# Kernel optimization log

Measured on AMD Instinct MI355X. Metric: run time of the kernel, lower is better.

Reference implementation:

```python
import jax, jax.numpy as jnp
import numpy as np

WS = 8        # window_size
HEAD_DIM = 32
KEYS = ["ln1_g", "ln1_b", "qkv_w", "qkv_b", "rpb", "proj_w", "proj_b",
        "ln2_g", "ln2_b", "w1", "b1", "w2", "b2"]


def _rel_bias(rpb, ws):
    # rpb: [h, 2ws-1, 2ws-1] -> bias [h, P, P] via relative coordinates
    coords = np.stack(np.meshgrid(np.arange(ws), np.arange(ws), indexing='ij'), -1).reshape(-1, 2)
    rel = coords[:, None, :] - coords[None, :, :] + ws - 1  # [P,P,2]
    return rpb[:, rel[..., 0], rel[..., 1]]


def _sw_mask(nh, nw, p, shift):
    # boolean mask [nW, P, P]; True = masked (cross-segment after cyclic shift)
    m = np.zeros((nh, nw, p, p, p, p), dtype=bool)
    s = p - shift
    m[-1, :, :s, :, s:, :] = True
    m[-1, :, s:, :, :s, :] = True
    m[:, -1, :, :s, :, s:] = True
    m[:, -1, :, s:, :, :s] = True
    return jnp.asarray(m.reshape(nh * nw, p * p, p * p))


def _ln(x, g, b):
    mu = x.mean(-1, keepdims=True)
    var = ((x - mu) ** 2).mean(-1, keepdims=True)
    return (x - mu) / jnp.sqrt(var + 1e-5) * g + b


def _wmsa(x, qkv_w, qkv_b, rpb, proj_w, proj_b, shifted):
    B, H, W, C = x.shape
    ws, hd = WS, HEAD_DIM
    h = C // hd
    shift = ws // 2
    if shifted:
        x = jnp.roll(x, (-shift, -shift), axis=(1, 2))
    nh, nw = H // ws, W // ws
    # window partition: [B, nW, P, C]
    xw = x.reshape(B, nh, ws, nw, ws, C).transpose(0, 1, 3, 2, 4, 5).reshape(B, nh * nw, ws * ws, C)
    qkv = xw @ qkv_w + qkv_b                               # [B,nW,P,3C]
    qkv = qkv.reshape(B, nh * nw, ws * ws, 3, h, hd)       # (3h,c) split -> first h heads = q
    q, k, v = qkv[..., 0, :, :], qkv[..., 1, :, :], qkv[..., 2, :, :]
    sim = jnp.einsum('bwphd,bwqhd->bhwpq', q, k) * (hd ** -0.5)
    sim = sim + _rel_bias(rpb, ws)[None, :, None]
    if shifted:
        mask = _sw_mask(nh, nw, ws, shift)                 # [nW,P,P]
        sim = jnp.where(mask[None, None], -jnp.inf, sim)
    probs = jax.nn.softmax(sim, axis=-1)
    out = jnp.einsum('bhwpq,bwqhd->bwphd', probs, v).reshape(B, nh * nw, ws * ws, C)
    out = out @ proj_w + proj_b
    out = out.reshape(B, nh, nw, ws, ws, C).transpose(0, 1, 3, 2, 4, 5).reshape(B, H, W, C)
    if shifted:
        out = jnp.roll(out, (shift, shift), axis=(1, 2))
    return out


def _block(x, p, shifted):
    x = x + _wmsa(_ln(x, p['ln1_g'], p['ln1_b']), p['qkv_w'], p['qkv_b'], p['rpb'],
                  p['proj_w'], p['proj_b'], shifted)
    y = _ln(x, p['ln2_g'], p['ln2_b'])
    y = jax.nn.gelu(y @ p['w1'] + p['b1'], approximate=False) @ p['w2'] + p['b2']
    return x + y


def setup_inputs() -> dict:
    B, C, H, W = 2, 192, 256, 256
    h = C // HEAD_DIM
    key = jax.random.key(0)
    ks = jax.random.split(key, 11)
    n = lambda k, shape: jax.random.normal(k, shape, jnp.float32) * 0.02
    inp = {"x": jax.random.normal(ks[0], (B, C, H, W), jnp.float32)}
    for i, pre in enumerate(("b1_", "b2_")):
        o = 1 + i * 5
        inp[pre + "ln1_g"] = jnp.ones((C,), jnp.float32)
        inp[pre + "ln1_b"] = jnp.zeros((C,), jnp.float32)
        inp[pre + "qkv_w"] = n(ks[o], (C, 3 * C))
        inp[pre + "qkv_b"] = jnp.zeros((3 * C,), jnp.float32)
        inp[pre + "rpb"] = n(ks[o + 1], (h, 2 * WS - 1, 2 * WS - 1))
        inp[pre + "proj_w"] = n(ks[o + 2], (C, C))
        inp[pre + "proj_b"] = jnp.zeros((C,), jnp.float32)
        inp[pre + "ln2_g"] = jnp.ones((C,), jnp.float32)
        inp[pre + "ln2_b"] = jnp.zeros((C,), jnp.float32)
        inp[pre + "w1"] = n(ks[o + 3], (C, 4 * C))
        inp[pre + "b1"] = jnp.zeros((4 * C,), jnp.float32)
        inp[pre + "w2"] = n(ks[o + 4], (4 * C, C))
        inp[pre + "b2"] = jnp.zeros((C,), jnp.float32)
    return inp


def reference(x, b1_ln1_g, b1_ln1_b, b1_qkv_w, b1_qkv_b, b1_rpb, b1_proj_w, b1_proj_b,
              b1_ln2_g, b1_ln2_b, b1_w1, b1_b1, b1_w2, b1_b2,
              b2_ln1_g, b2_ln1_b, b2_qkv_w, b2_qkv_b, b2_rpb, b2_proj_w, b2_proj_b,
              b2_ln2_g, b2_ln2_b, b2_w1, b2_b1, b2_w2, b2_b2):
    p1 = dict(zip(KEYS, (b1_ln1_g, b1_ln1_b, b1_qkv_w, b1_qkv_b, b1_rpb, b1_proj_w, b1_proj_b,
                         b1_ln2_g, b1_ln2_b, b1_w1, b1_b1, b1_w2, b1_b2)))
    p2 = dict(zip(KEYS, (b2_ln1_g, b2_ln1_b, b2_qkv_w, b2_qkv_b, b2_rpb, b2_proj_w, b2_proj_b,
                         b2_ln2_g, b2_ln2_b, b2_w1, b2_b1, b2_w2, b2_b2)))
    t = jnp.transpose(x, (0, 2, 3, 1))   # b c h w -> b h w c
    t = _block(t, p1, shifted=False)     # W block
    t = _block(t, p2, shifted=True)      # SW block
    return jnp.transpose(t, (0, 3, 1, 2))  # b h w c -> b c h w
```

## Files before the change

### kernel.cpp

```cpp
#include <hip/hip_runtime.h>
#include <math.h>

typedef unsigned short u16;
typedef u16 u16x8 __attribute__((ext_vector_type(8)));
typedef __bf16 bf16x8 __attribute__((ext_vector_type(8)));
typedef float f32x4 __attribute__((ext_vector_type(4)));

__device__ __forceinline__ u16 f2bf(float f) {
    union { float f; unsigned u; } v; v.f = f;
    unsigned r = v.u + 0x7fffu + ((v.u >> 16) & 1u);
    return (u16)(r >> 16);
}

__device__ __forceinline__ void gload16(const void* g, void* l) {
    __builtin_amdgcn_global_load_lds((const __attribute__((address_space(1))) void*)g,
                                     (__attribute__((address_space(3))) void*)l,
                                     16, 0, 0);
}

__device__ __forceinline__ float redsum16(float s) {
    s += __shfl_xor(s, 1, 64);
    s += __shfl_xor(s, 2, 64);
    s += __shfl_xor(s, 4, 64);
    s += __shfl_xor(s, 8, 64);
    return s;
}

__global__ __launch_bounds__(256) void tl_k(const float* __restrict__ in,
                                            const float* __restrict__ g,
                                            const float* __restrict__ b,
                                            float* __restrict__ xbuf,
                                            u16* __restrict__ lnbuf) {
    __shared__ float T[192][33];
    __shared__ float MU[32], RS[32];
    const int t = threadIdx.x;
    const int bid = blockIdx.x;
    const int bb = bid >> 11;
    const int s0 = (bid & 2047) * 32;
    const float* src = in + (size_t)bb * 192 * 65536 + s0;
    const int sx = t & 31, cg = t >> 5;
#pragma unroll
    for (int i = 0; i < 24; i++) {
        int c = cg + i * 8;
        T[c][sx] = src[(size_t)c * 65536 + sx];
    }
    __syncthreads();
    {
        const int tok = t >> 3, sub = t & 7;
        float s = 0.f;
#pragma unroll
        for (int i = 0; i < 24; i++) s += T[sub + i * 8][tok];
        s += __shfl_xor(s, 1, 64); s += __shfl_xor(s, 2, 64); s += __shfl_xor(s, 4, 64);
        float mu = s * (1.f / 192.f);
        float q = 0.f;
#pragma unroll
        for (int i = 0; i < 24; i++) { float d = T[sub + i * 8][tok] - mu; q += d * d; }
        q += __shfl_xor(q, 1, 64); q += __shfl_xor(q, 2, 64); q += __shfl_xor(q, 4, 64);
        if (sub == 0) { MU[tok] = mu; RS[tok] = rsqrtf(q * (1.f / 192.f) + 1e-5f); }
    }
    __syncthreads();
    const size_t tokG0 = (size_t)bb * 65536 + s0;
#pragma unroll
    for (int i = 0; i < 3; i++) {
        int chunk = i * 256 + t;
        int tk = chunk / 24;
        int c0 = (chunk - tk * 24) * 8;
        float mu = MU[tk], rs = RS[tk];
        f32x4 g0 = *(const f32x4*)&g[c0], g1 = *(const f32x4*)&g[c0 + 4];
        f32x4 b0 = *(const f32x4*)&b[c0], b1 = *(const f32x4*)&b[c0 + 4];
        u16x8 ov;
#pragma unroll
        for (int e = 0; e < 4; e++) ov[e] = f2bf((T[c0 + e][tk] - mu) * rs * g0[e] + b0[e]);
#pragma unroll
        for (int e = 0; e < 4; e++) ov[e + 4] = f2bf((T[c0 + 4 + e][tk] - mu) * rs * g1[e] + b1[e]);
        *(u16x8*)&lnbuf[(tokG0 + tk) * 192 + c0] = ov;
    }
#pragma unroll
    for (int i = 0; i < 6; i++) {
        int chunk = i * 256 + t;
        int tk = chunk / 48;
        int c0 = (chunk - tk * 48) * 4;
        f32x4 v;
#pragma unroll
        for (int e = 0; e < 4; e++) v[e] = T[c0 + e][tk];
        *(f32x4*)&xbuf[(tokG0 + tk) * 192 + c0] = v;
    }
}

__global__ __launch_bounds__(256) void transpose_out(const float* __restrict__ in,
                                                     float* __restrict__ out) {
    __shared__ float t[32][33];
    const int b = blockIdx.z;
    const int c0 = blockIdx.y * 32;
    const int s0 = blockIdx.x * 32;
    const int tx = threadIdx.x, ty = threadIdx.y;
    const float* src = in + (size_t)b * 65536 * 192;
    float* dst = out + (size_t)b * 192 * 65536;
#pragma unroll
    for (int k = 0; k < 4; k++)
        t[ty + k * 8][tx] = src[(size_t)(s0 + ty + k * 8) * 192 + c0 + tx];
    __syncthreads();
#pragma unroll
    for (int k = 0; k < 4; k++)
        dst[(size_t)(c0 + ty + k * 8) * 65536 + s0 + tx] = t[tx][ty + k * 8];
}

__global__ __launch_bounds__(256) void wtrans(const float* __restrict__ w,
                                              u16* __restrict__ wt, int K, int N) {
    int idx = blockIdx.x * 256 + threadIdx.x;
    if (idx >= K * N) return;
    int n = idx / K, k = idx % K;
    wt[idx] = f2bf(w[(size_t)k * N + n]);
}

template <int ACT>
__global__ __launch_bounds__(256, 4) void gemm_small(const u16* __restrict__ A,
                                                     const u16* __restrict__ Wt,
                                                     const float* __restrict__ bias,
                                                     u16* __restrict__ outb,
                                                     int N, int Nb) {
    __shared__ __align__(16) u16 Bs[64 * 192];
    const int t = threadIdx.x, l = t & 63, w = t >> 6;
    const int nwg = gridDim.x, q8 = nwg >> 3;
    const int wg = (blockIdx.x & 7) * q8 + (blockIdx.x >> 3);
    const int bn = wg % Nb, bm = wg / Nb;
    const size_t m0 = (size_t)bm * 128;
    const int n0 = bn * 64;
    const int lc = l & 15, lg = l >> 4;

#pragma unroll
    for (int r = 0; r < 6; r++) {
        int f = r * 2048 + t * 8;
        int row = f / 192;
        int c = ((f - row * 192) >> 3) ^ (row & 7);
        gload16(Wt + (size_t)(n0 + row) * 192 + c * 8, &Bs[f]);
    }
    const u16* ga = A + (m0 + w * 32 + lc) * 192 + lg * 8;
    bf16x8 af[6][2];
#pragma unroll
    for (int ks = 0; ks < 6; ks++)
#pragma unroll
        for (int tm = 0; tm < 2; tm++)
            af[ks][tm] = *(const bf16x8*)(ga + tm * 3072 + ks * 32);

    f32x4 acc[2][4] = {};
    __syncthreads();
#pragma unroll
    for (int ks = 0; ks < 6; ks++) {
        bf16x8 bfr[4];
#pragma unroll
        for (int tn = 0; tn < 4; tn++) {
            int row = tn * 16 + lc;
            int p = (ks * 4 + lg) ^ (row & 7);
            bfr[tn] = *(const bf16x8*)&Bs[row * 192 + p * 8];
        }
#pragma unroll
        for (int tm = 0; tm < 2; tm++)
#pragma unroll
            for (int tn = 0; tn < 4; tn++)
                acc[tm][tn] = __builtin_amdgcn_mfma_f32_16x16x32_bf16(af[ks][tm], bfr[tn],
                                                                     acc[tm][tn], 0, 0, 0);
    }
    float bv[4];
#pragma unroll
    for (int tn = 0; tn < 4; tn++) bv[tn] = bias[n0 + tn * 16 + lc];
    __syncthreads();
    u16* Ct = Bs;
#pragma unroll
    for (int tm = 0; tm < 2; tm++)
#pragma unroll
        for (int tn = 0; tn < 4; tn++)
#pragma unroll
            for (int r = 0; r < 4; r++) {
                int row = w * 32 + tm * 16 + (lg << 2) + r;
                float v = acc[tm][tn][r] + bv[tn];
                Ct[row * 72 + tn * 16 + lc] = f2bf(v);
            }
    __syncthreads();
#pragma unroll
    for (int i = 0; i < 4; i++) {
        int row = i * 32 + (t >> 3), seg = t & 7;
        *(u16x8*)&outb[(m0 + row) * (size_t)N + n0 + seg * 8] =
            *(const u16x8*)&Ct[row * 72 + seg * 8];
    }
}

__global__ __launch_bounds__(512, 4) void proj_ln_k(const u16* __restrict__ A,
                                                    const u16* __restrict__ Wt,
                                                    const float* __restrict__ bias,
                                                    float* __restrict__ res,
                                                    const float* __restrict__ g,
                                                    const float* __restrict__ b,
                                                    u16* __restrict__ lnout) {
    __shared__ __align__(16) u16 Bs[192 * 192];
    const int t = threadIdx.x, l = t & 63, w = t >> 6;
    const size_t m0 = (size_t)blockIdx.x * 128;
    const int lc = l & 15, lg = l >> 4;
#pragma unroll
    for (int r = 0; r < 9; r++) {
        int f = r * 4096 + t * 8;
        int row = f / 192;
        int c = ((f - row * 192) >> 3) ^ (row & 7);
        gload16(Wt + (size_t)row * 192 + c * 8, &Bs[f]);
    }
    const u16* ga = A + (m0 + w * 16 + lc) * 192 + lg * 8;
    bf16x8 af[6];
#pragma unroll
    for (int ks = 0; ks < 6; ks++) af[ks] = *(const bf16x8*)(ga + ks * 32);

    f32x4 acc[12] = {};
    __syncthreads();
#pragma unroll
    for (int ks = 0; ks < 6; ks++) {
#pragma unroll
        for (int grp = 0; grp < 3; grp++) {
            bf16x8 bfr[4];
#pragma unroll
            for (int tn = 0; tn < 4; tn++) {
                int row = (grp * 4 + tn) * 16 + lc;
                int p = (ks * 4 + lg) ^ (row & 7);
                bfr[tn] = *(const bf16x8*)&Bs[row * 192 + p * 8];
            }
#pragma unroll
            for (int tn = 0; tn < 4; tn++)
                acc[grp * 4 + tn] = __builtin_amdgcn_mfma_f32_16x16x32_bf16(af[ks], bfr[tn],
                                                                            acc[grp * 4 + tn], 0, 0, 0);
        }
    }
    float bv[12], gv[12], bb[12];
#pragma unroll
    for (int tn = 0; tn < 12; tn++) {
        bv[tn] = bias[tn * 16 + lc];
        gv[tn] = g[tn * 16 + lc];
        bb[tn] = b[tn * 16 + lc];
    }
#pragma unroll
    for (int r = 0; r < 4; r++) {
        int row = w * 16 + (lg << 2) + r;
        size_t base = (m0 + row) * 192;
        float v[12], s = 0.f;
#pragma unroll
        for (int tn = 0; tn < 12; tn++) {
            v[tn] = acc[tn][r] + bv[tn] + res[base + tn * 16 + lc];
            s += v[tn];
        }
        s = redsum16(s);
        float mu = s * (1.f / 192.f);
        float q = 0.f;
#pragma unroll
        for (int tn = 0; tn < 12; tn++) { float d = v[tn] - mu; q += d * d; }
        q = redsum16(q);
        float rstd = rsqrtf(q * (1.f / 192.f) + 1e-5f);
#pragma unroll
        for (int tn = 0; tn < 12; tn++) {
            res[base + tn * 16 + lc] = v[tn];
            lnout[base + tn * 16 + lc] = f2bf((v[tn] - mu) * rstd * gv[tn] + bb[tn]);
        }
    }
}

template <int DO_LN>
__global__ __launch_bounds__(512, 4) void mlp_fused(const u16* __restrict__ A,
                                                    const u16* __restrict__ W1t,
                                                    const float* __restrict__ b1,
                                                    const u16* __restrict__ W2t,
                                                    const float* __restrict__ b2,
                                                    float* __restrict__ res,
                                                    const float* __restrict__ g,
                                                    const float* __restrict__ bl,
                                                    u16* __restrict__ lnout) {
    __shared__ __align__(16) u16 W1s[32 * 192];
    __shared__ __align__(16) u16 W2s[192 * 32];
    __shared__ __align__(16) u16 Is[128 * 32];
    const int t = threadIdx.x, l = t & 63, w = t >> 6;
    const int nwg = gridDim.x, q8 = nwg >> 3;
    const int wg = (blockIdx.x & 7) * q8 + (blockIdx.x >> 3);
    const size_t m0 = (size_t)wg * 128;
    const int lc = l & 15, lg = l >> 4;

    const u16* ga = A + (m0 + w * 16 + lc) * 192 + lg * 8;
    bf16x8 af[6];
#pragma unroll
    for (int ks = 0; ks < 6; ks++) af[ks] = *(const bf16x8*)(ga + ks * 32);

#define STW1(c)                                                               \
    do {                                                                      \
        int f = t * 8;                                                        \
        int row = f / 192;                                                    \
        int cw = ((f - row * 192) >> 3) ^ (row & 7);                          \
        gload16(W1t + ((size_t)(c) * 32 + row) * 192 + cw * 8, &W1s[f]);      \
        if (t < 256) {                                                        \
            int f2 = (512 + t) * 8;                                           \
            int row2 = f2 / 192;                                              \
            int cw2 = ((f2 - row2 * 192) >> 3) ^ (row2 & 7);                  \
            gload16(W1t + ((size_t)(c) * 32 + row2) * 192 + cw2 * 8,          \
                    &W1s[f2]);                                                \
        }                                                                     \
    } while (0)
#define STW2(c)                                                               \
    do {                                                                      \
        int f = t * 8;                                                        \
        int row = f >> 5;                                                     \
        int cw = ((f >> 3) & 3) ^ ((row >> 1) & 3);                           \
        gload16(W2t + (size_t)row * 768 + (c) * 32 + cw * 8, &W2s[f]);        \
        if (t < 256) {                                                        \
            int f2 = (512 + t) * 8;                                           \
            int row2 = f2 >> 5;                                               \
            int cw2 = ((f2 >> 3) & 3) ^ ((row2 >> 1) & 3);                    \
            gload16(W2t + (size_t)row2 * 768 + (c) * 32 + cw2 * 8,            \
                    &W2s[f2]);                                                \
        }                                                                     \
    } while (0)

    f32x4 acc2[12] = {};
    STW1(0);
    STW2(0);
    __syncthreads();
#pragma unroll 1
    for (int c = 0; c < 24; c++) {
        f32x4 a1[2] = {};
#pragma unroll
        for (int ks = 0; ks < 6; ks++) {
            bf16x8 bfr[2];
#pragma unroll
            for (int tn = 0; tn < 2; tn++) {
                int row = tn * 16 + lc;
                int p = (ks * 4 + lg) ^ (row & 7);
                bfr[tn] = *(const bf16x8*)&W1s[row * 192 + p * 8];
            }
#pragma unroll
            for (int tn = 0; tn < 2; tn++)
                a1[tn] = __builtin_amdgcn_mfma_f32_16x16x32_bf16(af[ks], bfr[tn],
                                                                 a1[tn], 0, 0, 0);
        }
        float b1v[2];
#pragma unroll
        for (int tn = 0; tn < 2; tn++) b1v[tn] = b1[c * 32 + tn * 16 + lc];
#pragma unroll
        for (int tn = 0; tn < 2; tn++)
#pragma unroll
            for (int r = 0; r < 4; r++) {
                int row = w * 16 + (lg << 2) + r;
                int col = tn * 16 + lc;
                float x = a1[tn][r] + b1v[tn];
                float u = x * x;
                float y = x * fmaf(-0.07136031f, u, -1.5957691f);
                float v = x * __builtin_amdgcn_rcpf(1.0f + __expf(y));
                int cw = (col >> 3) ^ ((row >> 1) & 3);
                Is[row * 32 + cw * 8 + (col & 7)] = f2bf(v);
            }
        __syncthreads();
        if (c < 23) STW1(c + 1);
        bf16x8 a2;
        {
            int row = w * 16 + lc;
            int ch = lg ^ ((row >> 1) & 3);
            a2 = *(const bf16x8*)&Is[row * 32 + ch * 8];
        }
#pragma unroll
        for (int grp = 0; grp < 2; grp++) {
            bf16x8 b2f[6];
#pragma unroll
            for (int tn = 0; tn < 6; tn++) {
                int row = (grp * 6 + tn) * 16 + lc;
                int ch = lg ^ ((row >> 1) & 3);
                b2f[tn] = *(const bf16x8*)&W2s[row * 32 + ch * 8];
            }
#pragma unroll
            for (int tn = 0; tn < 6; tn++)
                acc2[grp * 6 + tn] = __builtin_amdgcn_mfma_f32_16x16x32_bf16(a2, b2f[tn],
                                                                            acc2[grp * 6 + tn], 0, 0, 0);
        }
        __syncthreads();
        if (c < 23) STW2(c + 1);
    }
#undef STW1
#undef STW2
    float bv[12];
#pragma unroll
    for (int tn = 0; tn < 12; tn++) bv[tn] = b2[tn * 16 + lc];
    float gv[12], bb[12];
    if (DO_LN) {
#pragma unroll
        for (int tn = 0; tn < 12; tn++) { gv[tn] = g[tn * 16 + lc]; bb[tn] = bl[tn * 16 + lc]; }
    }
#pragma unroll
    for (int r = 0; r < 4; r++) {
        int row = w * 16 + (lg << 2) + r;
        size_t base = (m0 + row) * 192;
        float v[12], s = 0.f;
#pragma unroll
        for (int tn = 0; tn < 12; tn++) {
            v[tn] = acc2[tn][r] + bv[tn] + res[base + tn * 16 + lc];
            s += v[tn];
        }
#pragma unroll
        for (int tn = 0; tn < 12; tn++) res[base + tn * 16 + lc] = v[tn];
        if (DO_LN) {
            s = redsum16(s);
            float mu = s * (1.f / 192.f);
            float q = 0.f;
#pragma unroll
            for (int tn = 0; tn < 12; tn++) { float d = v[tn] - mu; q += d * d; }
            q = redsum16(q);
            float rstd = rsqrtf(q * (1.f / 192.f) + 1e-5f);
#pragma unroll
            for (int tn = 0; tn < 12; tn++)
                lnout[base + tn * 16 + lc] = f2bf((v[tn] - mu) * rstd * gv[tn] + bb[tn]);
        }
    }
}

__global__ __launch_bounds__(64) void attn_k(const u16* __restrict__ qkv,
                                             const float* __restrict__ rpb,
                                             u16* __restrict__ aout, int shifted) {
    __shared__ __align__(16) u16 Vt[32][72];
    __shared__ __align__(16) u16 Ps[64][72];
    const int l = threadIdx.x;
    const int head = blockIdx.x;
    const int wy = blockIdx.y;
    const int b = wy >> 10, widx = wy & 1023;
    const int wh = widx >> 5, ww = widx & 31;
    const int soff = shifted ? 4 : 0;
    const int lc = l & 15;
    const int lg = l >> 4;

    {
        int i1 = l >> 3, j1 = l & 7;
        int hh = (wh * 8 + i1 + soff) & 255;
        int wc = (ww * 8 + j1 + soff) & 255;
        const u16* base = qkv + (((size_t)b * 256 + hh) * 256 + wc) * 576 + head * 32 + 384;
#pragma unroll
        for (int s = 0; s < 4; s++) {
            u16x8 v = *(const u16x8*)(base + s * 8);
#pragma unroll
            for (int e = 0; e < 8; e++) Vt[s * 8 + e][l] = v[e];
        }
    }

    bf16x8 qa[4], kb[4];
#pragma unroll
    for (int tm = 0; tm < 4; tm++) {
        int p = tm * 16 + lc;
        int pi = p >> 3, pj = p & 7;
        int hh = (wh * 8 + pi + soff) & 255;
        int wc = (ww * 8 + pj + soff) & 255;
        const u16* tp = qkv + (((size_t)b * 256 + hh) * 256 + wc) * 576 + head * 32;
        qa[tm] = *(const bf16x8*)(tp + lg * 8);
        kb[tm] = *(const bf16x8*)(tp + 192 + lg * 8);
    }

    f32x4 acc[4][4] = {};
    __builtin_amdgcn_s_setprio(1);
#pragma unroll
    for (int tm = 0; tm < 4; tm++)
#pragma unroll
        for (int tn = 0; tn < 4; tn++)
            acc[tm][tn] = __builtin_amdgcn_mfma_f32_16x16x32_bf16(qa[tm], kb[tn], acc[tm][tn], 0, 0, 0);
    __builtin_amdgcn_s_setprio(0);

    const float scale = 0.17677669529663687f;
    const float* rp = rpb + head * 225;
#pragma unroll
    for (int tm = 0; tm < 4; tm++) {
#pragma unroll
        for (int r = 0; r < 4; r++) {
            int p = tm * 16 + (lg << 2) + r;
            int pi = p >> 3, pj = p & 7;
            float sv[4];
#pragma unroll
            for (int tn = 0; tn < 4; tn++) {
                int qq = tn * 16 + lc;
                int qi = qq >> 3, qj = qq & 7;
                float xv = acc[tm][tn][r] * scale + rp[(pi - qi + 7) * 15 + (pj - qj + 7)];
                if (shifted) {
                    bool msk = (wh == 31 && ((pi < 4) != (qi < 4))) ||
                               (ww == 31 && ((pj < 4) != (qj < 4)));
                    if (msk) xv = -1e30f;
                }
                sv[tn] = xv;
            }
            float mx = fmaxf(fmaxf(sv[0], sv[1]), fmaxf(sv[2], sv[3]));
#pragma unroll
            for (int m = 1; m < 16; m <<= 1) mx = fmaxf(mx, __shfl_xor(mx, m, 64));
            float sum = 0.f;
#pragma unroll
            for (int tn = 0; tn < 4; tn++) { sv[tn] = __expf(sv[tn] - mx); sum += sv[tn]; }
#pragma unroll
            for (int m = 1; m < 16; m <<= 1) sum += __shfl_xor(sum, m, 64);
            float inv = 1.0f / sum;
#pragma unroll
            for (int tn = 0; tn < 4; tn++) Ps[p][tn * 16 + lc] = f2bf(sv[tn] * inv);
        }
    }
    __syncthreads();

    f32x4 o[4][2] = {};
    {
        bf16x8 pa[4], vb[2];
#pragma unroll
        for (int kk = 0; kk < 2; kk++) {
#pragma unroll
            for (int tm = 0; tm < 4; tm++) pa[tm] = *(const bf16x8*)&Ps[tm * 16 + lc][kk * 32 + lg * 8];
#pragma unroll
            for (int tn = 0; tn < 2; tn++) vb[tn] = *(const bf16x8*)&Vt[tn * 16 + lc][kk * 32 + lg * 8];
            __builtin_amdgcn_s_setprio(1);
#pragma unroll
            for (int tm = 0; tm < 4; tm++)
#pragma unroll
                for (int tn = 0; tn < 2; tn++)
                    o[tm][tn] = __builtin_amdgcn_mfma_f32_16x16x32_bf16(pa[tm], vb[tn], o[tm][tn], 0, 0, 0);
            __builtin_amdgcn_s_setprio(0);
        }
    }
#pragma unroll
    for (int tm = 0; tm < 4; tm++)
#pragma unroll
        for (int r = 0; r < 4; r++) {
            int p = tm * 16 + (lg << 2) + r;
            int pi = p >> 3, pj = p & 7;
            int h2 = (wh * 8 + pi + soff) & 255;
            int w2 = (ww * 8 + pj + soff) & 255;
            size_t t2 = ((size_t)b * 256 + h2) * 256 + w2;
#pragma unroll
            for (int tn = 0; tn < 2; tn++)
                aout[t2 * 192 + head * 32 + tn * 16 + lc] = f2bf(o[tm][tn][r]);
        }
}

extern "C" void kernel_launch(void* const* d_in, const int* in_sizes, int n_in,
                              void* d_out, int out_size, void* d_ws, size_t ws_size,
                              hipStream_t stream) {
    (void)in_sizes; (void)n_in; (void)out_size; (void)ws_size;
    const float* x_in = (const float*)d_in[0];

    char* ws = (char*)d_ws;
    float* xbuf = (float*)ws;
    u16* lnbuf = (u16*)(ws + 100663296);
    u16* big   = (u16*)(ws + 150994944);
    u16* wts   = (u16*)(ws + 352321536);

    u16* qkvt[2]; u16* projt[2]; u16* w1t[2]; u16* w2t[2];
    for (int bi = 0; bi < 2; bi++) {
        size_t base = (size_t)bi * 442368;
        qkvt[bi]  = wts + base;
        projt[bi] = wts + base + 110592;
        w1t[bi]   = wts + base + 147456;
        w2t[bi]   = wts + base + 294912;
    }

    for (int bi = 0; bi < 2; bi++) {
        const int base = 1 + bi * 13;
        wtrans<<<dim3((110592 + 255) / 256), 256, 0, stream>>>((const float*)d_in[base + 2],  qkvt[bi],  192, 576);
        wtrans<<<dim3((36864  + 255) / 256), 256, 0, stream>>>((const float*)d_in[base + 5],  projt[bi], 192, 192);
        wtrans<<<dim3((147456 + 255) / 256), 256, 0, stream>>>((const float*)d_in[base + 9],  w1t[bi],   192, 768);
        wtrans<<<dim3((147456 + 255) / 256), 256, 0, stream>>>((const float*)d_in[base + 11], w2t[bi],   768, 192);
    }

    tl_k<<<4096, 256, 0, stream>>>(x_in, (const float*)d_in[1], (const float*)d_in[2], xbuf, lnbuf);

    for (int bi = 0; bi < 2; bi++) {
        const int base = 1 + bi * 13;
        const float* qkv_b  = (const float*)d_in[base + 3];
        const float* rpb    = (const float*)d_in[base + 4];
        const float* proj_b = (const float*)d_in[base + 6];
        const float* ln2_g  = (const float*)d_in[base + 7];
        const float* ln2_b  = (const float*)d_in[base + 8];
        const float* b1     = (const float*)d_in[base + 10];
        const float* b2     = (const float*)d_in[base + 12];

        gemm_small<0><<<9216, 256, 0, stream>>>(lnbuf, qkvt[bi], qkv_b, big, 576, 9);
        attn_k<<<dim3(6, 2048), 64, 0, stream>>>(big, rpb, lnbuf, bi);
        proj_ln_k<<<1024, 512, 0, stream>>>(lnbuf, projt[bi], proj_b, xbuf, ln2_g, ln2_b, lnbuf);
        if (bi == 0) {
            mlp_fused<1><<<1024, 512, 0, stream>>>(lnbuf, w1t[bi], b1, w2t[bi], b2, xbuf,
                                                   (const float*)d_in[14], (const float*)d_in[15], lnbuf);
        } else {
            mlp_fused<0><<<1024, 512, 0, stream>>>(lnbuf, w1t[bi], b1, w2t[bi], b2, xbuf,
                                                   nullptr, nullptr, nullptr);
        }
    }

    transpose_out<<<dim3(2048, 6, 2), dim3(32, 8), 0, stream>>>(xbuf, (float*)d_out);
}
```

Measured before the change: 814.0 us.

## Fuse projection+LayerNorm into MLP kernel, keeping LN output in shared memory

Merges the attention output projection with residual add and LayerNorm into the fused MLP kernel. The normalized activations are written to a swizzled LDS buffer that aliases the projection weight tile, and the MLP reads its A fragments from there. This removes one kernel launch per block and the global write/read of the LN2 activations. The cost is a larger shared memory footprint and higher register pressure in a single kernel, which may reduce occupancy.

```diff
diff --git a/kernel.cpp b/kernel.cpp
--- a/kernel.cpp
+++ b/kernel.cpp
@@ -185,103 +185,99 @@
     }
 }
 
-__global__ __launch_bounds__(512, 4) void proj_ln_k(const u16* __restrict__ A,
-                                                    const u16* __restrict__ Wt,
-                                                    const float* __restrict__ bias,
-                                                    float* __restrict__ res,
-                                                    const float* __restrict__ g,
-                                                    const float* __restrict__ b,
-                                                    u16* __restrict__ lnout) {
-    __shared__ __align__(16) u16 Bs[192 * 192];
-    const int t = threadIdx.x, l = t & 63, w = t >> 6;
-    const size_t m0 = (size_t)blockIdx.x * 128;
-    const int lc = l & 15, lg = l >> 4;
-#pragma unroll
-    for (int r = 0; r < 9; r++) {
-        int f = r * 4096 + t * 8;
-        int row = f / 192;
-        int c = ((f - row * 192) >> 3) ^ (row & 7);
-        gload16(Wt + (size_t)row * 192 + c * 8, &Bs[f]);
-    }
-    const u16* ga = A + (m0 + w * 16 + lc) * 192 + lg * 8;
-    bf16x8 af[6];
-#pragma unroll
-    for (int ks = 0; ks < 6; ks++) af[ks] = *(const bf16x8*)(ga + ks * 32);
-
-    f32x4 acc[12] = {};
-    __syncthreads();
-#pragma unroll
-    for (int ks = 0; ks < 6; ks++) {
-#pragma unroll
-        for (int grp = 0; grp < 3; grp++) {
-            bf16x8 bfr[4];
-#pragma unroll
-            for (int tn = 0; tn < 4; tn++) {
-                int row = (grp * 4 + tn) * 16 + lc;
-                int p = (ks * 4 + lg) ^ (row & 7);
-                bfr[tn] = *(const bf16x8*)&Bs[row * 192 + p * 8];
-            }
-#pragma unroll
-            for (int tn = 0; tn < 4; tn++)
-                acc[grp * 4 + tn] = __builtin_amdgcn_mfma_f32_16x16x32_bf16(af[ks], bfr[tn],
-                                                                            acc[grp * 4 + tn], 0, 0, 0);
-        }
-    }
-    float bv[12], gv[12], bb[12];
-#pragma unroll
-    for (int tn = 0; tn < 12; tn++) {
-        bv[tn] = bias[tn * 16 + lc];
-        gv[tn] = g[tn * 16 + lc];
-        bb[tn] = b[tn * 16 + lc];
-    }
-#pragma unroll
-    for (int r = 0; r < 4; r++) {
-        int row = w * 16 + (lg << 2) + r;
-        size_t base = (m0 + row) * 192;
-        float v[12], s = 0.f;
-#pragma unroll
-        for (int tn = 0; tn < 12; tn++) {
-            v[tn] = acc[tn][r] + bv[tn] + res[base + tn * 16 + lc];
-            s += v[tn];
-        }
-        s = redsum16(s);
-        float mu = s * (1.f / 192.f);
-        float q = 0.f;
-#pragma unroll
-        for (int tn = 0; tn < 12; tn++) { float d = v[tn] - mu; q += d * d; }
-        q = redsum16(q);
-        float rstd = rsqrtf(q * (1.f / 192.f) + 1e-5f);
-#pragma unroll
-        for (int tn = 0; tn < 12; tn++) {
-            res[base + tn * 16 + lc] = v[tn];
-            lnout[base + tn * 16 + lc] = f2bf((v[tn] - mu) * rstd * gv[tn] + bb[tn]);
-        }
-    }
-}
-
 template <int DO_LN>
-__global__ __launch_bounds__(512, 4) void mlp_fused(const u16* __restrict__ A,
-                                                    const u16* __restrict__ W1t,
-                                                    const float* __restrict__ b1,
-                                                    const u16* __restrict__ W2t,
-                                                    const float* __restrict__ b2,
-                                                    float* __restrict__ res,
-                                                    const float* __restrict__ g,
-                                                    const float* __restrict__ bl,
-                                                    u16* __restrict__ lnout) {
-    __shared__ __align__(16) u16 W1s[32 * 192];
-    __shared__ __align__(16) u16 W2s[192 * 32];
-    __shared__ __align__(16) u16 Is[128 * 32];
+__global__ __launch_bounds__(512, 4) void proj_mlp(const u16* __restrict__ A,
+                                                   const u16* __restrict__ PWt,
+                                                   const float* __restrict__ pbias,
+                                                   const float* __restrict__ g2,
+                                                   const float* __restrict__ bl2,
+                                                   const u16* __restrict__ W1t,
+                                                   const float* __restrict__ b1,
+                                                   const u16* __restrict__ W2t,
+                                                   const float* __restrict__ b2,
+                                                   float* __restrict__ res,
+                                                   const float* __restrict__ gn,
+                                                   const float* __restrict__ bn,
+                                                   u16* __restrict__ lnout) {
+    __shared__ __align__(16) u16 SMEM[40960];
+    u16* Bs   = SMEM;
+    u16* ln2t = SMEM;
+    u16* W1s  = SMEM + 24576;
+    u16* W2s  = SMEM + 30720;
+    u16* Is   = SMEM + 36864;
     const int t = threadIdx.x, l = t & 63, w = t >> 6;
     const int nwg = gridDim.x, q8 = nwg >> 3;
     const int wg = (blockIdx.x & 7) * q8 + (blockIdx.x >> 3);
     const size_t m0 = (size_t)wg * 128;
     const int lc = l & 15, lg = l >> 4;
 
-    const u16* ga = A + (m0 + w * 16 + lc) * 192 + lg * 8;
-    bf16x8 af[6];
-#pragma unroll
-    for (int ks = 0; ks < 6; ks++) af[ks] = *(const bf16x8*)(ga + ks * 32);
+#pragma unroll
+    for (int r = 0; r < 9; r++) {
+        int f = r * 4096 + t * 8;
+        int row = f / 192;
+        int c = ((f - row * 192) >> 3) ^ (row & 7);
+        gload16(PWt + (size_t)row * 192 + c * 8, &Bs[f]);
+    }
+    {
+        const u16* ga = A + (m0 + w * 16 + lc) * 192 + lg * 8;
+        bf16x8 af[6];
+#pragma unroll
+        for (int ks = 0; ks < 6; ks++) af[ks] = *(const bf16x8*)(ga + ks * 32);
+
+        f32x4 acc[12] = {};
+        __syncthreads();
+#pragma unroll
+        for (int ks = 0; ks < 6; ks++) {
+#pragma unroll
+            for (int grp = 0; grp < 3; grp++) {
+                bf16x8 bfr[4];
+#pragma unroll
+                for (int tn = 0; tn < 4; tn++) {
+                    int row = (grp * 4 + tn) * 16 + lc;
+                    int p = (ks * 4 + lg) ^ (row & 7);
+                    bfr[tn] = *(const bf16x8*)&Bs[row * 192 + p * 8];
+                }
+#pragma unroll
+                for (int tn = 0; tn < 4; tn++)
+                    acc[grp * 4 + tn] = __builtin_amdgcn_mfma_f32_16x16x32_bf16(af[ks], bfr[tn],
+                                                                                acc[grp * 4 + tn], 0, 0, 0);
+            }
+        }
+        __syncthreads();
+
+        float pbv[12], gv[12], bb[12];
+#pragma unroll
+        for (int tn = 0; tn < 12; tn++) {
+            pbv[tn] = pbias[tn * 16 + lc];
+            gv[tn] = g2[tn * 16 + lc];
+            bb[tn] = bl2[tn * 16 + lc];
+        }
+#pragma unroll
+        for (int r = 0; r < 4; r++) {
+            int row = w * 16 + (lg << 2) + r;
+            size_t base = (m0 + row) * 192;
+            float v[12], s = 0.f;
+#pragma unroll
+            for (int tn = 0; tn < 12; tn++) {
+                v[tn] = acc[tn][r] + pbv[tn] + res[base + tn * 16 + lc];
+                s += v[tn];
+            }
+            s = redsum16(s);
+            float mu = s * (1.f / 192.f);
+            float q = 0.f;
+#pragma unroll
+            for (int tn = 0; tn < 12; tn++) { float d = v[tn] - mu; q += d * d; }
+            q = redsum16(q);
+            float rstd = rsqrtf(q * (1.f / 192.f) + 1e-5f);
+#pragma unroll
+            for (int tn = 0; tn < 12; tn++) {
+                res[base + tn * 16 + lc] = v[tn];
+                int col = tn * 16 + lc;
+                float lnv = (v[tn] - mu) * rstd * gv[tn] + bb[tn];
+                ln2t[row * 192 + (((col >> 3) ^ (row & 7)) << 3) + (col & 7)] = f2bf(lnv);
+            }
+        }
+    }
 
 #define STW1(c)                                                               \
     do {                                                                      \
@@ -312,10 +308,20 @@
         }                                                                     \
     } while (0)
 
-    f32x4 acc2[12] = {};
     STW1(0);
     STW2(0);
     __syncthreads();
+
+    bf16x8 af[6];
+    {
+        int row = w * 16 + lc;
+#pragma unroll
+        for (int ks = 0; ks < 6; ks++) {
+            int p = (ks * 4 + lg) ^ (row & 7);
+            af[ks] = *(const bf16x8*)&ln2t[row * 192 + p * 8];
+        }
+    }
+    f32x4 acc2[12] = {};
 #pragma unroll 1
     for (int c = 0; c < 24; c++) {
         f32x4 a1[2] = {};
@@ -376,13 +382,13 @@
     }
 #undef STW1
 #undef STW2
-    float bv[12];
-#pragma unroll
-    for (int tn = 0; tn < 12; tn++) bv[tn] = b2[tn * 16 + lc];
-    float gv[12], bb[12];
+    float bv2[12];
+#pragma unroll
+    for (int tn = 0; tn < 12; tn++) bv2[tn] = b2[tn * 16 + lc];
+    float gv2[12], bb2[12];
     if (DO_LN) {
 #pragma unroll
-        for (int tn = 0; tn < 12; tn++) { gv[tn] = g[tn * 16 + lc]; bb[tn] = bl[tn * 16 + lc]; }
+        for (int tn = 0; tn < 12; tn++) { gv2[tn] = gn[tn * 16 + lc]; bb2[tn] = bn[tn * 16 + lc]; }
     }
 #pragma unroll
     for (int r = 0; r < 4; r++) {
@@ -391,7 +397,7 @@
         float v[12], s = 0.f;
 #pragma unroll
         for (int tn = 0; tn < 12; tn++) {
-            v[tn] = acc2[tn][r] + bv[tn] + res[base + tn * 16 + lc];
+            v[tn] = acc2[tn][r] + bv2[tn] + res[base + tn * 16 + lc];
             s += v[tn];
         }
 #pragma unroll
@@ -406,7 +412,7 @@
             float rstd = rsqrtf(q * (1.f / 192.f) + 1e-5f);
 #pragma unroll
             for (int tn = 0; tn < 12; tn++)
-                lnout[base + tn * 16 + lc] = f2bf((v[tn] - mu) * rstd * gv[tn] + bb[tn]);
+                lnout[base + tn * 16 + lc] = f2bf((v[tn] - mu) * rstd * gv2[tn] + bb2[tn]);
         }
     }
 }
@@ -571,13 +577,14 @@
 
         gemm_small<0><<<9216, 256, 0, stream>>>(lnbuf, qkvt[bi], qkv_b, big, 576, 9);
         attn_k<<<dim3(6, 2048), 64, 0, stream>>>(big, rpb, lnbuf, bi);
-        proj_ln_k<<<1024, 512, 0, stream>>>(lnbuf, projt[bi], proj_b, xbuf, ln2_g, ln2_b, lnbuf);
         if (bi == 0) {
-            mlp_fused<1><<<1024, 512, 0, stream>>>(lnbuf, w1t[bi], b1, w2t[bi], b2, xbuf,
-                                                   (const float*)d_in[14], (const float*)d_in[15], lnbuf);
+            proj_mlp<1><<<1024, 512, 0, stream>>>(lnbuf, projt[bi], proj_b, ln2_g, ln2_b,
+                                                  w1t[bi], b1, w2t[bi], b2, xbuf,
+                                                  (const float*)d_in[14], (const float*)d_in[15], lnbuf);
         } else {
-            mlp_fused<0><<<1024, 512, 0, stream>>>(lnbuf, w1t[bi], b1, w2t[bi], b2, xbuf,
-                                                   nullptr, nullptr, nullptr);
+            proj_mlp<0><<<1024, 512, 0, stream>>>(lnbuf, projt[bi], proj_b, ln2_g, ln2_b,
+                                                  w1t[bi], b1, w2t[bi], b2, xbuf,
+                                                  nullptr, nullptr, nullptr);
         }
     }
 
```

Measured after the change: 823.4 us. No clear change (+1.2%).
